# Performance work log

Measured on AMD Instinct MI355X. Metric: run time of the kernel, lower is better.

## Reference

```python
import jax, jax.numpy as jnp
import numpy as np

N_NODES = 100000
N_EDGES = 1600000
D_FEAT = 64
N_CHANNELS = 64


def setup_inputs() -> dict:
    key = jax.random.key(0)
    k1, k2, k3, k4, k5, k6 = jax.random.split(key, 6)
    features = jax.random.normal(k1, (N_NODES, D_FEAT), dtype=jnp.float32)
    kernel = jax.random.normal(k2, (D_FEAT, N_CHANNELS), dtype=jnp.float32) * (1.0 / np.sqrt(D_FEAT))
    bias = jnp.zeros((N_CHANNELS,), dtype=jnp.float32)
    skip_weight = jax.random.normal(k3, (N_CHANNELS,), dtype=jnp.float32) * 0.1
    adj_rows = jax.random.randint(k4, (N_EDGES,), 0, N_NODES, dtype=jnp.int32)
    adj_cols = jax.random.randint(k5, (N_EDGES,), 0, N_NODES, dtype=jnp.int32)
    # normalized adjacency values (positive, ~1/degree scale)
    adj_vals = jax.random.uniform(k6, (N_EDGES,), dtype=jnp.float32) * (1.0 / 16.0)
    return {
        "features": features,
        "kernel": kernel,
        "bias": bias,
        "skip_weight": skip_weight,
        "adj_vals": adj_vals,
        "adj_rows": adj_rows,
        "adj_cols": adj_cols,
    }


def reference(features, kernel, bias, skip_weight, adj_vals, adj_rows, adj_cols):
    # dense transform: [N, d] @ [d, c] + [c]
    h = jnp.matmul(features, kernel) + bias
    # SpMM with COO adjacency: out[i] = sum_e{row[e]=i} vals[e] * h[col[e]]
    msg = adj_vals[:, None] * h[adj_cols]            # [E, c]
    agg = jax.ops.segment_sum(msg, adj_rows, num_segments=features.shape[0])
    # skip (broadcast add of skip_weight, per original code) + activation
    out = agg + skip_weight
    return jax.nn.selu(out)
```

## Files before the change

### kernel.cpp

```cpp
#include <hip/hip_runtime.h>
#include <math.h>

#define N_NODES   100000
#define N_EDGES   1600000
#define D_FEAT    64
#define N_CH      64

#define SELU_SCALE 1.0507009873554805f
#define SELU_ALPHA 1.6732632423543772f

#define SCAN_TPB   256
#define SCAN_ELEMS 1024
#define SCAN_NB    ((N_NODES + SCAN_ELEMS - 1) / SCAN_ELEMS)

#define G_ROWS_PER_WAVE 16
#define G_ROWS_PER_BLOCK (4 * G_ROWS_PER_WAVE)
#define NB_GEMM  ((N_NODES + G_ROWS_PER_BLOCK - 1) / G_ROWS_PER_BLOCK)
#define NB_SCAT4 ((N_EDGES / 4 + 255) / 256)

__device__ __forceinline__ void gemm_body(
    int gb,
    const float* __restrict__ feat,
    const float* __restrict__ W,
    const float* __restrict__ bias,
    float* __restrict__ h)
{
    int lane = threadIdx.x & 63;
    int wave = threadIdx.x >> 6;

    float Wc[D_FEAT];
    #pragma unroll
    for (int k = 0; k < D_FEAT; ++k) Wc[k] = W[k * N_CH + lane];
    float b = bias[lane];

    int row0 = (gb * 4 + wave) * G_ROWS_PER_WAVE;
    for (int r = 0; r < G_ROWS_PER_WAVE; ++r) {
        int row = row0 + r;
        if (row >= N_NODES) return;
        int row_u = __builtin_amdgcn_readfirstlane(row);
        const float* frow = feat + (size_t)row_u * D_FEAT;
        float a0 = b, a1 = 0.f, a2 = 0.f, a3 = 0.f;
        #pragma unroll
        for (int k = 0; k < D_FEAT; k += 4) {
            a0 = fmaf(frow[k + 0], Wc[k + 0], a0);
            a1 = fmaf(frow[k + 1], Wc[k + 1], a1);
            a2 = fmaf(frow[k + 2], Wc[k + 2], a2);
            a3 = fmaf(frow[k + 3], Wc[k + 3], a3);
        }
        h[row * N_CH + lane] = (a0 + a1) + (a2 + a3);
    }
}

__global__ __launch_bounds__(256) void zero_deg_kernel(int* __restrict__ deg)
{
    int i = blockIdx.x * 256 + threadIdx.x;
    if (i < N_NODES) deg[i] = 0;
}

__global__ __launch_bounds__(256) void degree_rank_kernel(
    const int* __restrict__ rows, int* __restrict__ deg, int* __restrict__ rank)
{
    int i = blockIdx.x * 256 + threadIdx.x;
    if (i < N_EDGES / 4) {
        const int4 r = reinterpret_cast<const int4*>(rows)[i];
        int4 k;
        k.x = atomicAdd(&deg[r.x], 1);
        k.y = atomicAdd(&deg[r.y], 1);
        k.z = atomicAdd(&deg[r.z], 1);
        k.w = atomicAdd(&deg[r.w], 1);
        reinterpret_cast<int4*>(rank)[i] = k;
    }
}

__global__ __launch_bounds__(SCAN_TPB) void scan1_kernel(
    const int* __restrict__ deg, int* __restrict__ row_start,
    int* __restrict__ partials)
{
    __shared__ int lds[SCAN_TPB];
    int t = threadIdx.x;
    int base = blockIdx.x * SCAN_ELEMS + t * 4;
    int v0 = (base + 0 < N_NODES) ? deg[base + 0] : 0;
    int v1 = (base + 1 < N_NODES) ? deg[base + 1] : 0;
    int v2 = (base + 2 < N_NODES) ? deg[base + 2] : 0;
    int v3 = (base + 3 < N_NODES) ? deg[base + 3] : 0;
    int s1 = v0, s2 = v0 + v1, s3 = v0 + v1 + v2, tot = v0 + v1 + v2 + v3;
    lds[t] = tot;
    __syncthreads();
    for (int off = 1; off < SCAN_TPB; off <<= 1) {
        int y = (t >= off) ? lds[t - off] : 0;
        __syncthreads();
        lds[t] += y;
        __syncthreads();
    }
    int texcl = (t > 0) ? lds[t - 1] : 0;
    if (t == SCAN_TPB - 1) partials[blockIdx.x] = lds[SCAN_TPB - 1];
    if (base + 0 < N_NODES) row_start[base + 0] = texcl;
    if (base + 1 < N_NODES) row_start[base + 1] = texcl + s1;
    if (base + 2 < N_NODES) row_start[base + 2] = texcl + s2;
    if (base + 3 < N_NODES) row_start[base + 3] = texcl + s3;
}

__global__ __launch_bounds__(128) void scan2_kernel(int* __restrict__ partials)
{
    __shared__ int lds[128];
    int t = threadIdx.x;
    lds[t] = (t < SCAN_NB) ? partials[t] : 0;
    __syncthreads();
    for (int off = 1; off < 128; off <<= 1) {
        int y = (t >= off) ? lds[t - off] : 0;
        __syncthreads();
        lds[t] += y;
        __syncthreads();
    }
    if (t < SCAN_NB) partials[t] = (t > 0) ? lds[t - 1] : 0;
}

__global__ __launch_bounds__(SCAN_TPB) void scan3_kernel(
    int* __restrict__ row_start, const int* __restrict__ partials)
{
    int t = threadIdx.x;
    int add = partials[blockIdx.x];
    int base = blockIdx.x * SCAN_ELEMS + t * 4;
    #pragma unroll
    for (int j = 0; j < 4; ++j) {
        int idx = base + j;
        if (idx < N_NODES) row_start[idx] += add;
    }
    if (blockIdx.x == 0 && t == 0) row_start[N_NODES] = N_EDGES;
}

__global__ __launch_bounds__(256) void scatter_pack_gemm_kernel(
    const int* __restrict__ rows, const int* __restrict__ rank,
    const int* __restrict__ cols, const float* __restrict__ vals,
    const int* __restrict__ row_start, unsigned long long* __restrict__ pack64,
    const float* __restrict__ feat, const float* __restrict__ W,
    const float* __restrict__ bias, float* __restrict__ h)
{
    if (blockIdx.x < NB_SCAT4) {
        int i = blockIdx.x * 256 + threadIdx.x;
        if (i < N_EDGES / 4) {
            const int4   r  = reinterpret_cast<const int4*>(rows)[i];
            const int4   rk = reinterpret_cast<const int4*>(rank)[i];
            const int4   c  = reinterpret_cast<const int4*>(cols)[i];
            const float4 v  = reinterpret_cast<const float4*>(vals)[i];
            unsigned long long p0 =
                ((unsigned long long)__float_as_uint(v.x) << 32) | (unsigned)c.x;
            unsigned long long p1 =
                ((unsigned long long)__float_as_uint(v.y) << 32) | (unsigned)c.y;
            unsigned long long p2 =
                ((unsigned long long)__float_as_uint(v.z) << 32) | (unsigned)c.z;
            unsigned long long p3 =
                ((unsigned long long)__float_as_uint(v.w) << 32) | (unsigned)c.w;
            __builtin_nontemporal_store(p0, &pack64[row_start[r.x] + rk.x]);
            __builtin_nontemporal_store(p1, &pack64[row_start[r.y] + rk.y]);
            __builtin_nontemporal_store(p2, &pack64[row_start[r.z] + rk.z]);
            __builtin_nontemporal_store(p3, &pack64[row_start[r.w] + rk.w]);
        }
    } else {
        gemm_body(blockIdx.x - NB_SCAT4, feat, W, bias, h);
    }
}

__global__ __launch_bounds__(256) void aggregate_pack_kernel(
    const int*   __restrict__ row_start,
    const uint2* __restrict__ pack,
    const float* __restrict__ h,
    const float* __restrict__ skip,
    float*       __restrict__ out)
{
    int pair = blockIdx.x * 4 + (threadIdx.x >> 6);
    int lane = threadIdx.x & 63;
    int r0 = pair * 2;
    if (r0 >= N_NODES) return;
    int r1 = r0 + 1;

    int s0 = row_start[r0], e0 = row_start[r0 + 1];
    int s1 = row_start[r1], e1 = row_start[r1 + 1];
    float skp = skip[lane];

    float a0 = 0.f, a1 = 0.f, a2 = 0.f, a3 = 0.f;
    float b0 = 0.f, b1 = 0.f, b2 = 0.f, b3 = 0.f;

    int j0 = s0, j1 = s1;
    while (j0 < e0 || j1 < e1) {
        int cnt0 = e0 - j0; cnt0 = cnt0 < 0 ? 0 : (cnt0 > 64 ? 64 : cnt0);
        int cnt1 = e1 - j1; cnt1 = cnt1 < 0 ? 0 : (cnt1 > 64 ? 64 : cnt1);
        uint2 p0 = make_uint2(0u, 0u), p1 = make_uint2(0u, 0u);
        if (lane < cnt0) p0 = pack[j0 + lane];
        if (lane < cnt1) p1 = pack[j1 + lane];
        int pc = cnt0 > cnt1 ? cnt0 : cnt1;
        pc = (pc + 3) & ~3;
        for (int k = 0; k < pc; k += 4) {
            int   c00 = __shfl((int)p0.x, k + 0, 64); float v00 = __shfl(__uint_as_float(p0.y), k + 0, 64);
            int   c10 = __shfl((int)p1.x, k + 0, 64); float v10 = __shfl(__uint_as_float(p1.y), k + 0, 64);
            int   c01 = __shfl((int)p0.x, k + 1, 64); float v01 = __shfl(__uint_as_float(p0.y), k + 1, 64);
            int   c11 = __shfl((int)p1.x, k + 1, 64); float v11 = __shfl(__uint_as_float(p1.y), k + 1, 64);
            int   c02 = __shfl((int)p0.x, k + 2, 64); float v02 = __shfl(__uint_as_float(p0.y), k + 2, 64);
            int   c12 = __shfl((int)p1.x, k + 2, 64); float v12 = __shfl(__uint_as_float(p1.y), k + 2, 64);
            int   c03 = __shfl((int)p0.x, k + 3, 64); float v03 = __shfl(__uint_as_float(p0.y), k + 3, 64);
            int   c13 = __shfl((int)p1.x, k + 3, 64); float v13 = __shfl(__uint_as_float(p1.y), k + 3, 64);
            a0 = fmaf(v00, h[c00 * N_CH + lane], a0);
            b0 = fmaf(v10, h[c10 * N_CH + lane], b0);
            a1 = fmaf(v01, h[c01 * N_CH + lane], a1);
            b1 = fmaf(v11, h[c11 * N_CH + lane], b1);
            a2 = fmaf(v02, h[c02 * N_CH + lane], a2);
            b2 = fmaf(v12, h[c12 * N_CH + lane], b2);
            a3 = fmaf(v03, h[c03 * N_CH + lane], a3);
            b3 = fmaf(v13, h[c13 * N_CH + lane], b3);
        }
        j0 += 64; j1 += 64;
    }
    float x0 = (a0 + a1) + (a2 + a3) + skp;
    float x1 = (b0 + b1) + (b2 + b3) + skp;
    float n0 = SELU_SCALE * SELU_ALPHA * expm1f(x0);
    float n1 = SELU_SCALE * SELU_ALPHA * expm1f(x1);
    out[r0 * N_CH + lane] = x0 > 0.f ? SELU_SCALE * x0 : n0;
    out[r1 * N_CH + lane] = x1 > 0.f ? SELU_SCALE * x1 : n1;
}

__global__ __launch_bounds__(256) void scatter_gemm_kernel(
    const int* __restrict__ rows, const int* __restrict__ rank,
    const int* __restrict__ row_start, int* __restrict__ perm,
    const float* __restrict__ feat, const float* __restrict__ W,
    const float* __restrict__ bias, float* __restrict__ h)
{
    if (blockIdx.x < NB_SCAT4) {
        int i = blockIdx.x * 256 + threadIdx.x;
        if (i < N_EDGES / 4) {
            const int4 r  = reinterpret_cast<const int4*>(rows)[i];
            const int4 rk = reinterpret_cast<const int4*>(rank)[i];
            int e0 = i * 4;
            perm[row_start[r.x] + rk.x] = e0 + 0;
            perm[row_start[r.y] + rk.y] = e0 + 1;
            perm[row_start[r.z] + rk.z] = e0 + 2;
            perm[row_start[r.w] + rk.w] = e0 + 3;
        }
    } else {
        gemm_body(blockIdx.x - NB_SCAT4, feat, W, bias, h);
    }
}

__global__ __launch_bounds__(256) void aggregate_kernel(
    const int*   __restrict__ row_start,
    const int*   __restrict__ perm,
    const int*   __restrict__ cols,
    const float* __restrict__ vals,
    const float* __restrict__ h,
    const float* __restrict__ skip,
    float*       __restrict__ out)
{
    int row  = blockIdx.x * 4 + (threadIdx.x >> 6);
    int lane = threadIdx.x & 63;
    if (row >= N_NODES) return;

    int s = row_start[row];
    int e = row_start[row + 1];

    float a0 = 0.f, a1 = 0.f, a2 = 0.f, a3 = 0.f;
    for (int j = s; j < e; j += 64) {
        int cnt = e - j;
        if (cnt > 64) cnt = 64;
        int   c = 0;
        float v = 0.f;
        if (lane < cnt) {
            int eid = perm[j + lane];
            c = cols[eid];
            v = vals[eid];
        }
        int pc = (cnt + 3) & ~3;
        for (int k = 0; k < pc; k += 4) {
            int   c0 = __shfl(c, k + 0, 64);
            float v0 = __shfl(v, k + 0, 64);
            int   c1 = __shfl(c, k + 1, 64);
            float v1 = __shfl(v, k + 1, 64);
            int   c2 = __shfl(c, k + 2, 64);
            float v2 = __shfl(v, k + 2, 64);
            int   c3 = __shfl(c, k + 3, 64);
            float v3 = __shfl(v, k + 3, 64);
            a0 = fmaf(v0, h[c0 * N_CH + lane], a0);
            a1 = fmaf(v1, h[c1 * N_CH + lane], a1);
            a2 = fmaf(v2, h[c2 * N_CH + lane], a2);
            a3 = fmaf(v3, h[c3 * N_CH + lane], a3);
        }
    }
    float x = (a0 + a1) + (a2 + a3) + skip[lane];
    float neg = SELU_SCALE * SELU_ALPHA * expm1f(x);
    out[row * N_CH + lane] = x > 0.f ? SELU_SCALE * x : neg;
}

__global__ __launch_bounds__(256) void gemm_only_kernel(
    const float* __restrict__ feat, const float* __restrict__ W,
    const float* __restrict__ bias, float* __restrict__ h)
{
    gemm_body(blockIdx.x, feat, W, bias, h);
}

__global__ __launch_bounds__(256) void init_out_kernel(
    float* __restrict__ out, const float* __restrict__ skip)
{
    int idx = blockIdx.x * 256 + threadIdx.x;
    if (idx < N_NODES * N_CH) out[idx] = skip[idx & (N_CH - 1)];
}

__global__ __launch_bounds__(256) void edge_kernel(
    const float* __restrict__ vals, const int* __restrict__ rows,
    const int* __restrict__ cols, const float* __restrict__ h,
    float* __restrict__ out)
{
    int e = blockIdx.x * 4 + (threadIdx.x >> 6);
    int lane = threadIdx.x & 63;
    if (e >= N_EDGES) return;
    int row = rows[e];
    int col = cols[e];
    float v = vals[e];
    atomicAdd(&out[row * N_CH + lane], v * h[col * N_CH + lane]);
}

__global__ __launch_bounds__(256) void selu_kernel(float* __restrict__ out)
{
    int idx = blockIdx.x * 256 + threadIdx.x;
    if (idx >= N_NODES * N_CH) return;
    float x = out[idx];
    float neg = SELU_SCALE * SELU_ALPHA * expm1f(x);
    out[idx] = x > 0.f ? SELU_SCALE * x : neg;
}

static inline size_t align256(size_t x) { return (x + 255) & ~(size_t)255; }

extern "C" void kernel_launch(void* const* d_in, const int* in_sizes, int n_in,
                              void* d_out, int out_size, void* d_ws, size_t ws_size,
                              hipStream_t stream)
{
    const float* features = (const float*)d_in[0];
    const float* W        = (const float*)d_in[1];
    const float* bias     = (const float*)d_in[2];
    const float* skip     = (const float*)d_in[3];
    const float* adj_vals = (const float*)d_in[4];
    const int*   adj_rows = (const int*)d_in[5];
    const int*   adj_cols = (const int*)d_in[6];
    float* out = (float*)d_out;

    char* ws = (char*)d_ws;
    size_t off = 0;
    float* h       = (float*)(ws + off);  off = align256(off + (size_t)N_NODES * N_CH * 4);
    int* row_start = (int*)(ws + off);    off = align256(off + (size_t)(N_NODES + 1) * 4);
    int* deg       = (int*)(ws + off);    off = align256(off + (size_t)N_NODES * 4);
    int* partials  = (int*)(ws + off);    off = align256(off + 128 * 4);
    int* rank      = (int*)(ws + off);    off = align256(off + (size_t)N_EDGES * 4);
    size_t need_perm = off + align256((size_t)N_EDGES * 4);
    size_t need_pack = off + align256((size_t)N_EDGES * 8);
    int*   perm = (int*)(ws + off);
    unsigned long long* pack64 = (unsigned long long*)(ws + off);
    uint2* pack = (uint2*)(ws + off);

    if (ws_size >= need_pack) {
        zero_deg_kernel<<<(N_NODES + 255) / 256, 256, 0, stream>>>(deg);
        degree_rank_kernel<<<NB_SCAT4, 256, 0, stream>>>(adj_rows, deg, rank);
        scan1_kernel<<<SCAN_NB, SCAN_TPB, 0, stream>>>(deg, row_start, partials);
        scan2_kernel<<<1, 128, 0, stream>>>(partials);
        scan3_kernel<<<SCAN_NB, SCAN_TPB, 0, stream>>>(row_start, partials);
        scatter_pack_gemm_kernel<<<NB_SCAT4 + NB_GEMM, 256, 0, stream>>>(
            adj_rows, rank, adj_cols, adj_vals, row_start, pack64,
            features, W, bias, h);
        aggregate_pack_kernel<<<(N_NODES / 2 + 3) / 4, 256, 0, stream>>>(
            row_start, pack, h, skip, out);
    } else if (ws_size >= need_perm) {
        zero_deg_kernel<<<(N_NODES + 255) / 256, 256, 0, stream>>>(deg);
        degree_rank_kernel<<<NB_SCAT4, 256, 0, stream>>>(adj_rows, deg, rank);
        scan1_kernel<<<SCAN_NB, SCAN_TPB, 0, stream>>>(deg, row_start, partials);
        scan2_kernel<<<1, 128, 0, stream>>>(partials);
        scan3_kernel<<<SCAN_NB, SCAN_TPB, 0, stream>>>(row_start, partials);
        scatter_gemm_kernel<<<NB_SCAT4 + NB_GEMM, 256, 0, stream>>>(
            adj_rows, rank, row_start, perm, features, W, bias, h);
        aggregate_kernel<<<(N_NODES + 3) / 4, 256, 0, stream>>>(
            row_start, perm, adj_cols, adj_vals, h, skip, out);
    } else {
        gemm_only_kernel<<<NB_GEMM, 256, 0, stream>>>(features, W, bias, h);
        init_out_kernel<<<(N_NODES * N_CH + 255) / 256, 256, 0, stream>>>(out, skip);
        edge_kernel<<<(N_EDGES + 3) / 4, 256, 0, stream>>>(
            adj_vals, adj_rows, adj_cols, h, out);
        selu_kernel<<<(N_NODES * N_CH + 255) / 256, 256, 0, stream>>>(out);
    }
}
```

Measured before the change: 312.0 us.

## Store transformed features as bf16 and fuse GEMM with degree counting

The dense transform now writes h as bf16 (round-to-nearest-even), and the aggregation kernel gathers bf16 values and widens them to fp32 before accumulating. This halves the bytes moved by the random-access gather. The GEMM also moves from the scatter kernel into the degree/rank kernel, so the scatter pass runs alone. The unused perm fallback path is removed. The cost is reduced precision in h, which may affect tolerance checks.

```diff
diff --git a/kernel.cpp b/kernel.cpp
--- a/kernel.cpp
+++ b/kernel.cpp
@@ -18,12 +18,23 @@
 #define NB_GEMM  ((N_NODES + G_ROWS_PER_BLOCK - 1) / G_ROWS_PER_BLOCK)
 #define NB_SCAT4 ((N_EDGES / 4 + 255) / 256)
 
-__device__ __forceinline__ void gemm_body(
+__device__ __forceinline__ unsigned short f2bf_rne(float x)
+{
+    unsigned b = __float_as_uint(x);
+    unsigned r = (b + 0x7FFFu + ((b >> 16) & 1u)) >> 16;
+    return (unsigned short)r;
+}
+__device__ __forceinline__ float bf2f(unsigned short u)
+{
+    return __uint_as_float(((unsigned)u) << 16);
+}
+
+__device__ __forceinline__ void gemm_body_bf16(
     int gb,
     const float* __restrict__ feat,
     const float* __restrict__ W,
     const float* __restrict__ bias,
-    float* __restrict__ h)
+    unsigned short* __restrict__ h_bf)
 {
     int lane = threadIdx.x & 63;
     int wave = threadIdx.x >> 6;
@@ -47,7 +58,7 @@
             a2 = fmaf(frow[k + 2], Wc[k + 2], a2);
             a3 = fmaf(frow[k + 3], Wc[k + 3], a3);
         }
-        h[row * N_CH + lane] = (a0 + a1) + (a2 + a3);
+        h_bf[row * N_CH + lane] = f2bf_rne((a0 + a1) + (a2 + a3));
     }
 }
 
@@ -57,18 +68,24 @@
     if (i < N_NODES) deg[i] = 0;
 }
 
-__global__ __launch_bounds__(256) void degree_rank_kernel(
-    const int* __restrict__ rows, int* __restrict__ deg, int* __restrict__ rank)
-{
-    int i = blockIdx.x * 256 + threadIdx.x;
-    if (i < N_EDGES / 4) {
-        const int4 r = reinterpret_cast<const int4*>(rows)[i];
-        int4 k;
-        k.x = atomicAdd(&deg[r.x], 1);
-        k.y = atomicAdd(&deg[r.y], 1);
-        k.z = atomicAdd(&deg[r.z], 1);
-        k.w = atomicAdd(&deg[r.w], 1);
-        reinterpret_cast<int4*>(rank)[i] = k;
+__global__ __launch_bounds__(256) void degree_rank_gemm_kernel(
+    const int* __restrict__ rows, int* __restrict__ deg, int* __restrict__ rank,
+    const float* __restrict__ feat, const float* __restrict__ W,
+    const float* __restrict__ bias, unsigned short* __restrict__ h_bf)
+{
+    if (blockIdx.x < NB_SCAT4) {
+        int i = blockIdx.x * 256 + threadIdx.x;
+        if (i < N_EDGES / 4) {
+            const int4 r = reinterpret_cast<const int4*>(rows)[i];
+            int4 k;
+            k.x = atomicAdd(&deg[r.x], 1);
+            k.y = atomicAdd(&deg[r.y], 1);
+            k.z = atomicAdd(&deg[r.z], 1);
+            k.w = atomicAdd(&deg[r.w], 1);
+            reinterpret_cast<int4*>(rank)[i] = k;
+        }
+    } else {
+        gemm_body_bf16(blockIdx.x - NB_SCAT4, feat, W, bias, h_bf);
     }
 }
 
@@ -129,42 +146,36 @@
     if (blockIdx.x == 0 && t == 0) row_start[N_NODES] = N_EDGES;
 }
 
-__global__ __launch_bounds__(256) void scatter_pack_gemm_kernel(
+__global__ __launch_bounds__(256) void scatter_pack_kernel(
     const int* __restrict__ rows, const int* __restrict__ rank,
     const int* __restrict__ cols, const float* __restrict__ vals,
-    const int* __restrict__ row_start, unsigned long long* __restrict__ pack64,
-    const float* __restrict__ feat, const float* __restrict__ W,
-    const float* __restrict__ bias, float* __restrict__ h)
-{
-    if (blockIdx.x < NB_SCAT4) {
-        int i = blockIdx.x * 256 + threadIdx.x;
-        if (i < N_EDGES / 4) {
-            const int4   r  = reinterpret_cast<const int4*>(rows)[i];
-            const int4   rk = reinterpret_cast<const int4*>(rank)[i];
-            const int4   c  = reinterpret_cast<const int4*>(cols)[i];
-            const float4 v  = reinterpret_cast<const float4*>(vals)[i];
-            unsigned long long p0 =
-                ((unsigned long long)__float_as_uint(v.x) << 32) | (unsigned)c.x;
-            unsigned long long p1 =
-                ((unsigned long long)__float_as_uint(v.y) << 32) | (unsigned)c.y;
-            unsigned long long p2 =
-                ((unsigned long long)__float_as_uint(v.z) << 32) | (unsigned)c.z;
-            unsigned long long p3 =
-                ((unsigned long long)__float_as_uint(v.w) << 32) | (unsigned)c.w;
-            __builtin_nontemporal_store(p0, &pack64[row_start[r.x] + rk.x]);
-            __builtin_nontemporal_store(p1, &pack64[row_start[r.y] + rk.y]);
-            __builtin_nontemporal_store(p2, &pack64[row_start[r.z] + rk.z]);
-            __builtin_nontemporal_store(p3, &pack64[row_start[r.w] + rk.w]);
-        }
-    } else {
-        gemm_body(blockIdx.x - NB_SCAT4, feat, W, bias, h);
+    const int* __restrict__ row_start, unsigned long long* __restrict__ pack64)
+{
+    int i = blockIdx.x * 256 + threadIdx.x;
+    if (i < N_EDGES / 4) {
+        const int4   r  = reinterpret_cast<const int4*>(rows)[i];
+        const int4   rk = reinterpret_cast<const int4*>(rank)[i];
+        const int4   c  = reinterpret_cast<const int4*>(cols)[i];
+        const float4 v  = reinterpret_cast<const float4*>(vals)[i];
+        unsigned long long p0 =
+            ((unsigned long long)__float_as_uint(v.x) << 32) | (unsigned)c.x;
+        unsigned long long p1 =
+            ((unsigned long long)__float_as_uint(v.y) << 32) | (unsigned)c.y;
+        unsigned long long p2 =
+            ((unsigned long long)__float_as_uint(v.z) << 32) | (unsigned)c.z;
+        unsigned long long p3 =
+            ((unsigned long long)__float_as_uint(v.w) << 32) | (unsigned)c.w;
+        __builtin_nontemporal_store(p0, &pack64[row_start[r.x] + rk.x]);
+        __builtin_nontemporal_store(p1, &pack64[row_start[r.y] + rk.y]);
+        __builtin_nontemporal_store(p2, &pack64[row_start[r.z] + rk.z]);
+        __builtin_nontemporal_store(p3, &pack64[row_start[r.w] + rk.w]);
     }
 }
 
 __global__ __launch_bounds__(256) void aggregate_pack_kernel(
     const int*   __restrict__ row_start,
     const uint2* __restrict__ pack,
-    const float* __restrict__ h,
+    const unsigned short* __restrict__ h_bf,
     const float* __restrict__ skip,
     float*       __restrict__ out)
 {
@@ -199,14 +210,22 @@
             int   c12 = __shfl((int)p1.x, k + 2, 64); float v12 = __shfl(__uint_as_float(p1.y), k + 2, 64);
             int   c03 = __shfl((int)p0.x, k + 3, 64); float v03 = __shfl(__uint_as_float(p0.y), k + 3, 64);
             int   c13 = __shfl((int)p1.x, k + 3, 64); float v13 = __shfl(__uint_as_float(p1.y), k + 3, 64);
-            a0 = fmaf(v00, h[c00 * N_CH + lane], a0);
-            b0 = fmaf(v10, h[c10 * N_CH + lane], b0);
-            a1 = fmaf(v01, h[c01 * N_CH + lane], a1);
-            b1 = fmaf(v11, h[c11 * N_CH + lane], b1);
-            a2 = fmaf(v02, h[c02 * N_CH + lane], a2);
-            b2 = fmaf(v12, h[c12 * N_CH + lane], b2);
-            a3 = fmaf(v03, h[c03 * N_CH + lane], a3);
-            b3 = fmaf(v13, h[c13 * N_CH + lane], b3);
+            float g00 = bf2f(h_bf[c00 * N_CH + lane]);
+            float g10 = bf2f(h_bf[c10 * N_CH + lane]);
+            float g01 = bf2f(h_bf[c01 * N_CH + lane]);
+            float g11 = bf2f(h_bf[c11 * N_CH + lane]);
+            float g02 = bf2f(h_bf[c02 * N_CH + lane]);
+            float g12 = bf2f(h_bf[c12 * N_CH + lane]);
+            float g03 = bf2f(h_bf[c03 * N_CH + lane]);
+            float g13 = bf2f(h_bf[c13 * N_CH + lane]);
+            a0 = fmaf(v00, g00, a0);
+            b0 = fmaf(v10, g10, b0);
+            a1 = fmaf(v01, g01, a1);
+            b1 = fmaf(v11, g11, b1);
+            a2 = fmaf(v02, g02, a2);
+            b2 = fmaf(v12, g12, b2);
+            a3 = fmaf(v03, g03, a3);
+            b3 = fmaf(v13, g13, b3);
         }
         j0 += 64; j1 += 64;
     }
@@ -218,81 +237,32 @@
     out[r1 * N_CH + lane] = x1 > 0.f ? SELU_SCALE * x1 : n1;
 }
 
-__global__ __launch_bounds__(256) void scatter_gemm_kernel(
-    const int* __restrict__ rows, const int* __restrict__ rank,
-    const int* __restrict__ row_start, int* __restrict__ perm,
-    const float* __restrict__ feat, const float* __restrict__ W,
-    const float* __restrict__ bias, float* __restrict__ h)
-{
-    if (blockIdx.x < NB_SCAT4) {
-        int i = blockIdx.x * 256 + threadIdx.x;
-        if (i < N_EDGES / 4) {
-            const int4 r  = reinterpret_cast<const int4*>(rows)[i];
-            const int4 rk = reinterpret_cast<const int4*>(rank)[i];
-            int e0 = i * 4;
-            perm[row_start[r.x] + rk.x] = e0 + 0;
-            perm[row_start[r.y] + rk.y] = e0 + 1;
-            perm[row_start[r.z] + rk.z] = e0 + 2;
-            perm[row_start[r.w] + rk.w] = e0 + 3;
-        }
-    } else {
-        gemm_body(blockIdx.x - NB_SCAT4, feat, W, bias, h);
-    }
-}
-
-__global__ __launch_bounds__(256) void aggregate_kernel(
-    const int*   __restrict__ row_start,
-    const int*   __restrict__ perm,
-    const int*   __restrict__ cols,
-    const float* __restrict__ vals,
-    const float* __restrict__ h,
-    const float* __restrict__ skip,
-    float*       __restrict__ out)
-{
-    int row  = blockIdx.x * 4 + (threadIdx.x >> 6);
-    int lane = threadIdx.x & 63;
-    if (row >= N_NODES) return;
-
-    int s = row_start[row];
-    int e = row_start[row + 1];
-
-    float a0 = 0.f, a1 = 0.f, a2 = 0.f, a3 = 0.f;
-    for (int j = s; j < e; j += 64) {
-        int cnt = e - j;
-        if (cnt > 64) cnt = 64;
-        int   c = 0;
-        float v = 0.f;
-        if (lane < cnt) {
-            int eid = perm[j + lane];
-            c = cols[eid];
-            v = vals[eid];
-        }
-        int pc = (cnt + 3) & ~3;
-        for (int k = 0; k < pc; k += 4) {
-            int   c0 = __shfl(c, k + 0, 64);
-            float v0 = __shfl(v, k + 0, 64);
-            int   c1 = __shfl(c, k + 1, 64);
-            float v1 = __shfl(v, k + 1, 64);
-            int   c2 = __shfl(c, k + 2, 64);
-            float v2 = __shfl(v, k + 2, 64);
-            int   c3 = __shfl(c, k + 3, 64);
-            float v3 = __shfl(v, k + 3, 64);
-            a0 = fmaf(v0, h[c0 * N_CH + lane], a0);
-            a1 = fmaf(v1, h[c1 * N_CH + lane], a1);
-            a2 = fmaf(v2, h[c2 * N_CH + lane], a2);
-            a3 = fmaf(v3, h[c3 * N_CH + lane], a3);
-        }
-    }
-    float x = (a0 + a1) + (a2 + a3) + skip[lane];
-    float neg = SELU_SCALE * SELU_ALPHA * expm1f(x);
-    out[row * N_CH + lane] = x > 0.f ? SELU_SCALE * x : neg;
-}
-
 __global__ __launch_bounds__(256) void gemm_only_kernel(
     const float* __restrict__ feat, const float* __restrict__ W,
     const float* __restrict__ bias, float* __restrict__ h)
 {
-    gemm_body(blockIdx.x, feat, W, bias, h);
+    int lane = threadIdx.x & 63;
+    int wave = threadIdx.x >> 6;
+    float Wc[D_FEAT];
+    #pragma unroll
+    for (int k = 0; k < D_FEAT; ++k) Wc[k] = W[k * N_CH + lane];
+    float b = bias[lane];
+    int row0 = (blockIdx.x * 4 + wave) * G_ROWS_PER_WAVE;
+    for (int r = 0; r < G_ROWS_PER_WAVE; ++r) {
+        int row = row0 + r;
+        if (row >= N_NODES) return;
+        int row_u = __builtin_amdgcn_readfirstlane(row);
+        const float* frow = feat + (size_t)row_u * D_FEAT;
+        float a0 = b, a1 = 0.f, a2 = 0.f, a3 = 0.f;
+        #pragma unroll
+        for (int k = 0; k < D_FEAT; k += 4) {
+            a0 = fmaf(frow[k + 0], Wc[k + 0], a0);
+            a1 = fmaf(frow[k + 1], Wc[k + 1], a1);
+            a2 = fmaf(frow[k + 2], Wc[k + 2], a2);
+            a3 = fmaf(frow[k + 3], Wc[k + 3], a3);
+        }
+        h[row * N_CH + lane] = (a0 + a1) + (a2 + a3);
+    }
 }
 
 __global__ __launch_bounds__(256) void init_out_kernel(
@@ -342,39 +312,29 @@
 
     char* ws = (char*)d_ws;
     size_t off = 0;
-    float* h       = (float*)(ws + off);  off = align256(off + (size_t)N_NODES * N_CH * 4);
-    int* row_start = (int*)(ws + off);    off = align256(off + (size_t)(N_NODES + 1) * 4);
-    int* deg       = (int*)(ws + off);    off = align256(off + (size_t)N_NODES * 4);
-    int* partials  = (int*)(ws + off);    off = align256(off + 128 * 4);
-    int* rank      = (int*)(ws + off);    off = align256(off + (size_t)N_EDGES * 4);
-    size_t need_perm = off + align256((size_t)N_EDGES * 4);
-    size_t need_pack = off + align256((size_t)N_EDGES * 8);
-    int*   perm = (int*)(ws + off);
+    unsigned short* h_bf = (unsigned short*)(ws + off);
+    off = align256(off + (size_t)N_NODES * N_CH * 2);
+    int* row_start = (int*)(ws + off);  off = align256(off + (size_t)(N_NODES + 1) * 4);
+    int* deg       = (int*)(ws + off);  off = align256(off + (size_t)N_NODES * 4);
+    int* partials  = (int*)(ws + off);  off = align256(off + 128 * 4);
+    int* rank      = (int*)(ws + off);  off = align256(off + (size_t)N_EDGES * 4);
     unsigned long long* pack64 = (unsigned long long*)(ws + off);
     uint2* pack = (uint2*)(ws + off);
-
-    if (ws_size >= need_pack) {
+    size_t need = off + align256((size_t)N_EDGES * 8);
+
+    if (ws_size >= need) {
         zero_deg_kernel<<<(N_NODES + 255) / 256, 256, 0, stream>>>(deg);
-        degree_rank_kernel<<<NB_SCAT4, 256, 0, stream>>>(adj_rows, deg, rank);
+        degree_rank_gemm_kernel<<<NB_SCAT4 + NB_GEMM, 256, 0, stream>>>(
+            adj_rows, deg, rank, features, W, bias, h_bf);
         scan1_kernel<<<SCAN_NB, SCAN_TPB, 0, stream>>>(deg, row_start, partials);
         scan2_kernel<<<1, 128, 0, stream>>>(partials);
         scan3_kernel<<<SCAN_NB, SCAN_TPB, 0, stream>>>(row_start, partials);
-        scatter_pack_gemm_kernel<<<NB_SCAT4 + NB_GEMM, 256, 0, stream>>>(
-            adj_rows, rank, adj_cols, adj_vals, row_start, pack64,
-            features, W, bias, h);
+        scatter_pack_kernel<<<NB_SCAT4, 256, 0, stream>>>(
+            adj_rows, rank, adj_cols, adj_vals, row_start, pack64);
         aggregate_pack_kernel<<<(N_NODES / 2 + 3) / 4, 256, 0, stream>>>(
-            row_start, pack, h, skip, out);
-    } else if (ws_size >= need_perm) {
-        zero_deg_kernel<<<(N_NODES + 255) / 256, 256, 0, stream>>>(deg);
-        degree_rank_kernel<<<NB_SCAT4, 256, 0, stream>>>(adj_rows, deg, rank);
-        scan1_kernel<<<SCAN_NB, SCAN_TPB, 0, stream>>>(deg, row_start, partials);
-        scan2_kernel<<<1, 128, 0, stream>>>(partials);
-        scan3_kernel<<<SCAN_NB, SCAN_TPB, 0, stream>>>(row_start, partials);
-        scatter_gemm_kernel<<<NB_SCAT4 + NB_GEMM, 256, 0, stream>>>(
-            adj_rows, rank, row_start, perm, features, W, bias, h);
-        aggregate_kernel<<<(N_NODES + 3) / 4, 256, 0, stream>>>(
-            row_start, perm, adj_cols, adj_vals, h, skip, out);
+            row_start, pack, h_bf, skip, out);
     } else {
+        float* h = (float*)d_ws;
         gemm_only_kernel<<<NB_GEMM, 256, 0, stream>>>(features, W, bias, h);
         init_out_kernel<<<(N_NODES * N_CH + 255) / 256, 256, 0, stream>>>(out, skip);
         edge_kernel<<<(N_EDGES + 3) / 4, 256, 0, stream>>>(
```

Result: faster. 301.8 us (-3.3%).
